# Performance work log

Measured on AMD Instinct MI355X. Metric: run time of the kernel, lower is better.

## Reference

```python
import jax, jax.numpy as jnp
import numpy as np

N_RAYS, N_SAMPLES, HIDDEN, N_VOXELS = 8192, 256, 64, 1000


def setup_inputs() -> dict:
    key = jax.random.key(0)
    ks = jax.random.split(key, 10)
    ray_start = jax.random.normal(ks[0], (N_RAYS, 3), jnp.float32)
    ray_dir = jax.random.normal(ks[1], (N_RAYS, 3), jnp.float32)
    ray_dir = ray_dir / jnp.linalg.norm(ray_dir, axis=-1, keepdims=True)
    # monotonically increasing depths along each ray
    sampled_depth = jnp.sort(jax.random.uniform(ks[2], (N_RAYS, N_SAMPLES), jnp.float32) * 4.0 + 0.5, axis=-1)
    sampled_dists = jax.random.uniform(ks[3], (N_RAYS, N_SAMPLES), jnp.float32) * 0.02 + 1e-3
    sampled_idx = jax.random.randint(ks[4], (N_RAYS, N_SAMPLES), -333, N_VOXELS).astype(jnp.int64)
    W1 = jax.random.normal(ks[5], (3, HIDDEN), jnp.float32) * 0.5
    b1 = jnp.zeros((HIDDEN,), jnp.float32)
    w_sigma = jax.random.normal(ks[6], (HIDDEN,), jnp.float32) * 0.5
    W_rgb = jax.random.normal(ks[7], (HIDDEN, 3), jnp.float32) * 0.5
    W_dir = jax.random.normal(ks[8], (3, 3), jnp.float32) * 0.5
    b_rgb = jnp.zeros((3,), jnp.float32)
    return {"ray_start": ray_start, "ray_dir": ray_dir, "sampled_depth": sampled_depth,
            "sampled_dists": sampled_dists, "sampled_idx": sampled_idx,
            "W1": W1, "b1": b1, "w_sigma": w_sigma, "W_rgb": W_rgb, "W_dir": W_dir, "b_rgb": b_rgb}


def _volume_render(ray_start, ray_dir, sampled_depth, sampled_dists, sampled_idx,
                   W1, b1, w_sigma, W_rgb, W_dir, b_rgb):
    # sampled_xyz = ray(ray_start, ray_dir, depth)
    xyz = ray_start[:, None, :] + ray_dir[:, None, :] * sampled_depth[..., None]  # [N,P,3]
    h = jax.nn.relu(jnp.einsum('npi,ih->nph', xyz, W1) + b1)                      # [N,P,H]
    sigma = jnp.einsum('nph,h->np', h, w_sigma)                                   # [N,P]
    rgb = jax.nn.sigmoid(jnp.einsum('nph,hc->npc', h, W_rgb)
                         + jnp.einsum('ni,ic->nc', ray_dir, W_dir)[:, None, :] + b_rgb)  # [N,P,3]
    mask = (sampled_idx != -1).astype(sigma.dtype)                                # [N,P]
    # free_energy = relu(sigma) * dists * 7.0, scattered back with zeros at misses
    free_energy = jax.nn.relu(sigma) * sampled_dists * 7.0 * mask
    shifted = jnp.concatenate([jnp.zeros_like(free_energy[:, :1]), free_energy[:, :-1]], axis=-1)
    a = 1.0 - jnp.exp(-free_energy)
    b = jnp.exp(-jnp.cumsum(shifted, axis=-1))
    probs = a * b                                                                 # [N,P]
    depths = jnp.sum(sampled_depth * probs, axis=-1)                              # [N]
    missed = 1.0 - jnp.sum(probs, axis=-1)                                        # [N]
    colors = jnp.sum(rgb * probs[..., None], axis=-2)                             # [N,3]
    return jnp.concatenate([colors, depths[:, None], missed[:, None], probs], axis=-1)  # [N, 3+1+1+P]


def reference(ray_start, ray_dir, sampled_depth, sampled_dists, sampled_idx,
              W1, b1, w_sigma, W_rgb, W_dir, b_rgb):
    return _volume_render(ray_start, ray_dir, sampled_depth, sampled_dists, sampled_idx,
                          W1, b1, w_sigma, W_rgb, W_dir, b_rgb)
```

## Files before the change

### kernel.cpp

```cpp
#include <hip/hip_runtime.h>

#define NRAYS 8192
#define NS    256
#define HID   64
#define NPAIR 32
#define RPB   8

typedef _Float16 f16x2 __attribute__((ext_vector_type(2)));
typedef _Float16 f16x8 __attribute__((ext_vector_type(8)));
typedef float    f32x4 __attribute__((ext_vector_type(4)));

static __device__ __forceinline__ f16x2 mk2(float a, float b) {
    f16x2 v; v.x = (_Float16)a; v.y = (_Float16)b; return v;
}

struct __align__(8) AB2 { f16x2 A, B; };
union AFrag { f16x8 v; f16x2 h[4]; };

__global__ __launch_bounds__(256, 4) void vr_kernel(
    const float* __restrict__ ray_start,
    const float* __restrict__ ray_dir,
    const float* __restrict__ sampled_depth,
    const float* __restrict__ sampled_dists,
    const int*   __restrict__ sampled_idx,
    const float* __restrict__ W1,
    const float* __restrict__ b1,
    const float* __restrict__ w_sigma,
    const float* __restrict__ W_rgb,
    const float* __restrict__ W_dir,
    const float* __restrict__ b_rgb,
    float* __restrict__ out)
{
    __shared__ AB2   sAB[RPB][NPAIR];
    __shared__ f16x2 sDep[RPB][NS];
    __shared__ __align__(16) float sOut[4][4][264];

    const int t = threadIdx.x;

    {
        const int rr  = t >> 5;
        const int k   = t & (NPAIR - 1);
        const int ray = blockIdx.x * RPB + rr;
        const float ox = ray_start[ray*3+0], oy = ray_start[ray*3+1], oz = ray_start[ray*3+2];
        const float dx = ray_dir[ray*3+0],  dy = ray_dir[ray*3+1],  dz = ray_dir[ray*3+2];
        const int h0 = 2*k, h1 = 2*k + 1;
        const float u0 = W1[h0], u1 = W1[HID + h0], u2 = W1[2*HID + h0];
        const float v0 = W1[h1], v1 = W1[HID + h1], v2 = W1[2*HID + h1];
        const float A0 = fmaf(u0, ox, fmaf(u1, oy, fmaf(u2, oz, b1[h0])));
        const float B0 = fmaf(u0, dx, fmaf(u1, dy, u2 * dz));
        const float A1 = fmaf(v0, ox, fmaf(v1, oy, fmaf(v2, oz, b1[h1])));
        const float B1 = fmaf(v0, dx, fmaf(v1, dy, v2 * dz));
        AB2 e; e.A = mk2(A0, A1); e.B = mk2(B0, B1);
        sAB[rr][k] = e;
    }
    {
        const int rr  = t >> 5;
        const int i   = t & 31;
        const int ray = blockIdx.x * RPB + rr;
        const size_t base = (size_t)ray * NS + (size_t)i * 8;
        const float4 d0 = ((const float4*)(sampled_depth + base))[0];
        const float4 d1 = ((const float4*)(sampled_depth + base))[1];
        f16x2* dst = &sDep[rr][i*8];
        dst[0] = mk2(d0.x, d0.x); dst[1] = mk2(d0.y, d0.y);
        dst[2] = mk2(d0.z, d0.z); dst[3] = mk2(d0.w, d0.w);
        dst[4] = mk2(d1.x, d1.x); dst[5] = mk2(d1.y, d1.y);
        dst[6] = mk2(d1.z, d1.z); dst[7] = mk2(d1.w, d1.w);
    }

    const int lane = t & 63;
    const int wave = t >> 6;
    const int col  = lane & 15;
    const int g    = lane >> 4;

    f16x8 bf0, bf1;
#pragma unroll
    for (int e = 0; e < 8; ++e) {
        const int u0 = g*8 + e, u1 = 32 + g*8 + e;
        float v0 = 0.f, v1 = 0.f;
        if (col == 0)     { v0 = w_sigma[u0];           v1 = w_sigma[u1]; }
        else if (col < 4) { v0 = W_rgb[u0*3 + (col-1)]; v1 = W_rgb[u1*3 + (col-1)]; }
        bf0[e] = (_Float16)v0; bf1[e] = (_Float16)v1;
    }

    const f16x2 zero2 = mk2(0.f, 0.f);
    const f32x4 zacc  = {0.f, 0.f, 0.f, 0.f};
    const int sb = 4*lane;

#pragma unroll 1
    for (int q = 0; q < 2; ++q) {
        const int r   = wave*2 + q;
        const int ray = blockIdx.x * RPB + r;

        AB2 c0[4], c1[4];
#pragma unroll
        for (int d = 0; d < 4; ++d) {
            c0[d] = sAB[r][4*g + d];
            c1[d] = sAB[r][16 + 4*g + d];
        }

        const float ddx = ray_dir[ray*3+0], ddy = ray_dir[ray*3+1], ddz = ray_dir[ray*3+2];
        const float dwr = fmaf(ddx, W_dir[0], fmaf(ddy, W_dir[3], fmaf(ddz, W_dir[6], b_rgb[0])));
        const float dwg = fmaf(ddx, W_dir[1], fmaf(ddy, W_dir[4], fmaf(ddz, W_dir[7], b_rgb[1])));
        const float dwb = fmaf(ddx, W_dir[2], fmaf(ddy, W_dir[5], fmaf(ddz, W_dir[8], b_rgb[2])));

        float4 dpt, dsv; int4 vid;

#pragma unroll
        for (int p = 0; p < 2; ++p) {
            f32x4 acc[8];
#pragma unroll
            for (int b = 0; b < 8; ++b) acc[b] = zacc;

#pragma unroll
            for (int b = 0; b < 8; ++b) {
                const int bb = 8*p + b;
                const f16x2 t2 = sDep[r][16*bb + col];
                AFrag a0, a1;
#pragma unroll
                for (int d = 0; d < 4; ++d) {
                    a0.h[d] = __builtin_elementwise_max(
                        __builtin_elementwise_fma(c0[d].B, t2, c0[d].A), zero2);
                    a1.h[d] = __builtin_elementwise_max(
                        __builtin_elementwise_fma(c1[d].B, t2, c1[d].A), zero2);
                }
                acc[b] = __builtin_amdgcn_mfma_f32_16x16x32_f16(a0.v, bf0, acc[b], 0, 0, 0);
                acc[b] = __builtin_amdgcn_mfma_f32_16x16x32_f16(a1.v, bf1, acc[b], 0, 0, 0);
            }

            if (col < 4) {
#pragma unroll
                for (int b = 0; b < 8; ++b) {
                    const int bb = 8*p + b;
                    float4 v; v.x = acc[b][0]; v.y = acc[b][1]; v.z = acc[b][2]; v.w = acc[b][3];
                    *(float4*)&sOut[wave][col][16*bb + 4*g] = v;
                }
            }

            if (p == 0) {
                const size_t rb = (size_t)ray * NS + (size_t)sb;
                dpt = *(const float4*)(sampled_depth + rb);
                dsv = *(const float4*)(sampled_dists + rb);
                vid = *(const int4*)(sampled_idx + rb);
            }
        }

        const float4 sg  = *(const float4*)&sOut[wave][0][sb];
        const float4 cr4 = *(const float4*)&sOut[wave][1][sb];
        const float4 cg4 = *(const float4*)&sOut[wave][2][sb];
        const float4 cb4 = *(const float4*)&sOut[wave][3][sb];

        const float sigA[4] = {sg.x,  sg.y,  sg.z,  sg.w};
        const float crA[4]  = {cr4.x, cr4.y, cr4.z, cr4.w};
        const float cgA[4]  = {cg4.x, cg4.y, cg4.z, cg4.w};
        const float cbA[4]  = {cb4.x, cb4.y, cb4.z, cb4.w};
        const float dptA[4] = {dpt.x, dpt.y, dpt.z, dpt.w};
        const float dsvA[4] = {dsv.x, dsv.y, dsv.z, dsv.w};
        const int   vidA[4] = {vid.x, vid.y, vid.z, vid.w};

        float c[4]; float run = 0.f;
#pragma unroll
        for (int j = 0; j < 4; ++j) {
            float f = fmaxf(sigA[j], 0.f) * dsvA[j] * 7.0f;
            if (vidA[j] == -1) f = 0.f;
            run += f; c[j] = run;
        }

        float tot = run;
#pragma unroll
        for (int off = 1; off < 64; off <<= 1) {
            const float v = __shfl_up(tot, off, 64);
            if (lane >= off) tot += v;
        }
        const float base = tot - run;

        float Eprev = __expf(-base);
        float prob[4];
        float sS = 0.f, sD = 0.f, sR = 0.f, sG = 0.f, sB = 0.f;
#pragma unroll
        for (int j = 0; j < 4; ++j) {
            const float Ej = __expf(-(base + c[j]));
            const float p  = Eprev - Ej;
            Eprev = Ej;
            prob[j] = p;
            const float rr2 = __builtin_amdgcn_rcpf(1.f + __expf(-(crA[j] + dwr)));
            const float gg2 = __builtin_amdgcn_rcpf(1.f + __expf(-(cgA[j] + dwg)));
            const float bb2 = __builtin_amdgcn_rcpf(1.f + __expf(-(cbA[j] + dwb)));
            sS += p;
            sD = fmaf(dptA[j], p, sD);
            sR = fmaf(rr2, p, sR);
            sG = fmaf(gg2, p, sG);
            sB = fmaf(bb2, p, sB);
        }

#pragma unroll
        for (int off = 32; off >= 1; off >>= 1) {
            sS += __shfl_xor(sS, off);
            sD += __shfl_xor(sD, off);
            sR += __shfl_xor(sR, off);
            sG += __shfl_xor(sG, off);
            sB += __shfl_xor(sB, off);
        }

        float* orow = out + (size_t)ray * (NS + 5);
#pragma unroll
        for (int j = 0; j < 4; ++j)
            orow[5 + sb + j] = prob[j];

        if (lane == 0) {
            orow[0] = sR;
            orow[1] = sG;
            orow[2] = sB;
            orow[3] = sD;
            orow[4] = 1.f - sS;
        }
    }
}

extern "C" void kernel_launch(void* const* d_in, const int* in_sizes, int n_in,
                              void* d_out, int out_size, void* d_ws, size_t ws_size,
                              hipStream_t stream)
{
    vr_kernel<<<NRAYS / RPB, 256, 0, stream>>>(
        (const float*)d_in[0],
        (const float*)d_in[1],
        (const float*)d_in[2],
        (const float*)d_in[3],
        (const int*)  d_in[4],
        (const float*)d_in[5],
        (const float*)d_in[6],
        (const float*)d_in[7],
        (const float*)d_in[8],
        (const float*)d_in[9],
        (const float*)d_in[10],
        (float*)d_out);
}
```

Baseline: 100.8 us.

## Merge per-ray epilogues into one half-wave-per-ray pass after both MFMA phases

Each wave now runs the MFMA phase for both of its rays first and keeps both results in a doubled shared output buffer. It then does a single epilogue in which each half-wave handles one ray with 8 samples per lane, so the scan and reduction use 32-lane shuffles. This removes one serialized epilogue per wave and halves the shuffle depth. Depth is stored in shared memory as packed f16 and broadcast in registers, and the per-ray direction term is computed once up front. The cost is more shared memory and more registers, which can lower occupancy.

New measurement: 100.7 us. Within noise of the previous version (-0.1%).

```diff
diff --git a/kernel.cpp b/kernel.cpp
--- a/kernel.cpp
+++ b/kernel.cpp
@@ -31,9 +31,9 @@
     const float* __restrict__ b_rgb,
     float* __restrict__ out)
 {
-    __shared__ AB2   sAB[RPB][NPAIR];
-    __shared__ f16x2 sDep[RPB][NS];
-    __shared__ __align__(16) float sOut[4][4][264];
+    __shared__ AB2 sAB[RPB][NPAIR];
+    __shared__ __align__(16) _Float16 sDepF[RPB][NS];
+    __shared__ __align__(16) float sOut[4][2][4][264];
 
     const int t = threadIdx.x;
 
@@ -60,17 +60,22 @@
         const size_t base = (size_t)ray * NS + (size_t)i * 8;
         const float4 d0 = ((const float4*)(sampled_depth + base))[0];
         const float4 d1 = ((const float4*)(sampled_depth + base))[1];
-        f16x2* dst = &sDep[rr][i*8];
-        dst[0] = mk2(d0.x, d0.x); dst[1] = mk2(d0.y, d0.y);
-        dst[2] = mk2(d0.z, d0.z); dst[3] = mk2(d0.w, d0.w);
-        dst[4] = mk2(d1.x, d1.x); dst[5] = mk2(d1.y, d1.y);
-        dst[6] = mk2(d1.z, d1.z); dst[7] = mk2(d1.w, d1.w);
+        f16x8 pk;
+        pk[0] = (_Float16)d0.x; pk[1] = (_Float16)d0.y;
+        pk[2] = (_Float16)d0.z; pk[3] = (_Float16)d0.w;
+        pk[4] = (_Float16)d1.x; pk[5] = (_Float16)d1.y;
+        pk[6] = (_Float16)d1.z; pk[7] = (_Float16)d1.w;
+        *(f16x8*)&sDepF[rr][i*8] = pk;
     }
 
     const int lane = t & 63;
     const int wave = t >> 6;
     const int col  = lane & 15;
     const int g    = lane >> 4;
+
+    const int hl   = lane & 31;
+    const int rq   = lane >> 5;
+    const int eray = blockIdx.x * RPB + wave*2 + rq;
 
     f16x8 bf0, bf1;
 #pragma unroll
@@ -82,14 +87,21 @@
         bf0[e] = (_Float16)v0; bf1[e] = (_Float16)v1;
     }
 
+    float dwr, dwg, dwb;
+    {
+        const float ddx = ray_dir[eray*3+0], ddy = ray_dir[eray*3+1], ddz = ray_dir[eray*3+2];
+        dwr = fmaf(ddx, W_dir[0], fmaf(ddy, W_dir[3], fmaf(ddz, W_dir[6], b_rgb[0])));
+        dwg = fmaf(ddx, W_dir[1], fmaf(ddy, W_dir[4], fmaf(ddz, W_dir[7], b_rgb[1])));
+        dwb = fmaf(ddx, W_dir[2], fmaf(ddy, W_dir[5], fmaf(ddz, W_dir[8], b_rgb[2])));
+    }
+
     const f16x2 zero2 = mk2(0.f, 0.f);
     const f32x4 zacc  = {0.f, 0.f, 0.f, 0.f};
-    const int sb = 4*lane;
-
-#pragma unroll 1
-    for (int q = 0; q < 2; ++q) {
-        const int r   = wave*2 + q;
-        const int ray = blockIdx.x * RPB + r;
+
+    float4 dptE0, dptE1, dsvE0, dsvE1; int4 vidE0, vidE1;
+
+    auto run_main = [&](int q, bool pf) {
+        const int r = wave*2 + q;
 
         AB2 c0[4], c1[4];
 #pragma unroll
@@ -98,12 +110,7 @@
             c1[d] = sAB[r][16 + 4*g + d];
         }
 
-        const float ddx = ray_dir[ray*3+0], ddy = ray_dir[ray*3+1], ddz = ray_dir[ray*3+2];
-        const float dwr = fmaf(ddx, W_dir[0], fmaf(ddy, W_dir[3], fmaf(ddz, W_dir[6], b_rgb[0])));
-        const float dwg = fmaf(ddx, W_dir[1], fmaf(ddy, W_dir[4], fmaf(ddz, W_dir[7], b_rgb[1])));
-        const float dwb = fmaf(ddx, W_dir[2], fmaf(ddy, W_dir[5], fmaf(ddz, W_dir[8], b_rgb[2])));
-
-        float4 dpt, dsv; int4 vid;
+        const unsigned short* sd = (const unsigned short*)sDepF[r];
 
 #pragma unroll
         for (int p = 0; p < 2; ++p) {
@@ -114,7 +121,9 @@
 #pragma unroll
             for (int b = 0; b < 8; ++b) {
                 const int bb = 8*p + b;
-                const f16x2 t2 = sDep[r][16*bb + col];
+                const unsigned int raw = sd[16*bb + col];
+                const unsigned int bits = (raw << 16) | raw;
+                const f16x2 t2 = __builtin_bit_cast(f16x2, bits);
                 AFrag a0, a1;
 #pragma unroll
                 for (int d = 0; d < 4; ++d) {
@@ -132,87 +141,98 @@
                 for (int b = 0; b < 8; ++b) {
                     const int bb = 8*p + b;
                     float4 v; v.x = acc[b][0]; v.y = acc[b][1]; v.z = acc[b][2]; v.w = acc[b][3];
-                    *(float4*)&sOut[wave][col][16*bb + 4*g] = v;
+                    *(float4*)&sOut[wave][q][col][16*bb + 4*g] = v;
                 }
             }
 
-            if (p == 0) {
-                const size_t rb = (size_t)ray * NS + (size_t)sb;
-                dpt = *(const float4*)(sampled_depth + rb);
-                dsv = *(const float4*)(sampled_dists + rb);
-                vid = *(const int4*)(sampled_idx + rb);
+            if (pf && p == 0) {
+                const size_t erb = (size_t)eray * NS + (size_t)hl * 8;
+                dptE0 = ((const float4*)(sampled_depth + erb))[0];
+                dptE1 = ((const float4*)(sampled_depth + erb))[1];
+                dsvE0 = ((const float4*)(sampled_dists + erb))[0];
+                dsvE1 = ((const float4*)(sampled_dists + erb))[1];
+                vidE0 = ((const int4*)(sampled_idx + erb))[0];
+                vidE1 = ((const int4*)(sampled_idx + erb))[1];
             }
         }
-
-        const float4 sg  = *(const float4*)&sOut[wave][0][sb];
-        const float4 cr4 = *(const float4*)&sOut[wave][1][sb];
-        const float4 cg4 = *(const float4*)&sOut[wave][2][sb];
-        const float4 cb4 = *(const float4*)&sOut[wave][3][sb];
-
-        const float sigA[4] = {sg.x,  sg.y,  sg.z,  sg.w};
-        const float crA[4]  = {cr4.x, cr4.y, cr4.z, cr4.w};
-        const float cgA[4]  = {cg4.x, cg4.y, cg4.z, cg4.w};
-        const float cbA[4]  = {cb4.x, cb4.y, cb4.z, cb4.w};
-        const float dptA[4] = {dpt.x, dpt.y, dpt.z, dpt.w};
-        const float dsvA[4] = {dsv.x, dsv.y, dsv.z, dsv.w};
-        const int   vidA[4] = {vid.x, vid.y, vid.z, vid.w};
-
-        float c[4]; float run = 0.f;
-#pragma unroll
-        for (int j = 0; j < 4; ++j) {
-            float f = fmaxf(sigA[j], 0.f) * dsvA[j] * 7.0f;
-            if (vidA[j] == -1) f = 0.f;
-            run += f; c[j] = run;
-        }
-
-        float tot = run;
-#pragma unroll
-        for (int off = 1; off < 64; off <<= 1) {
-            const float v = __shfl_up(tot, off, 64);
-            if (lane >= off) tot += v;
-        }
-        const float base = tot - run;
-
-        float Eprev = __expf(-base);
-        float prob[4];
-        float sS = 0.f, sD = 0.f, sR = 0.f, sG = 0.f, sB = 0.f;
-#pragma unroll
-        for (int j = 0; j < 4; ++j) {
-            const float Ej = __expf(-(base + c[j]));
-            const float p  = Eprev - Ej;
-            Eprev = Ej;
-            prob[j] = p;
-            const float rr2 = __builtin_amdgcn_rcpf(1.f + __expf(-(crA[j] + dwr)));
-            const float gg2 = __builtin_amdgcn_rcpf(1.f + __expf(-(cgA[j] + dwg)));
-            const float bb2 = __builtin_amdgcn_rcpf(1.f + __expf(-(cbA[j] + dwb)));
-            sS += p;
-            sD = fmaf(dptA[j], p, sD);
-            sR = fmaf(rr2, p, sR);
-            sG = fmaf(gg2, p, sG);
-            sB = fmaf(bb2, p, sB);
-        }
-
-#pragma unroll
-        for (int off = 32; off >= 1; off >>= 1) {
-            sS += __shfl_xor(sS, off);
-            sD += __shfl_xor(sD, off);
-            sR += __shfl_xor(sR, off);
-            sG += __shfl_xor(sG, off);
-            sB += __shfl_xor(sB, off);
-        }
-
-        float* orow = out + (size_t)ray * (NS + 5);
-#pragma unroll
-        for (int j = 0; j < 4; ++j)
-            orow[5 + sb + j] = prob[j];
-
-        if (lane == 0) {
-            orow[0] = sR;
-            orow[1] = sG;
-            orow[2] = sB;
-            orow[3] = sD;
-            orow[4] = 1.f - sS;
-        }
+    };
+
+    run_main(0, false);
+    run_main(1, true);
+
+    const int sb = 8*hl;
+    const float4 sg0 = *(const float4*)&sOut[wave][rq][0][sb];
+    const float4 sg1 = *(const float4*)&sOut[wave][rq][0][sb+4];
+    const float4 cr0 = *(const float4*)&sOut[wave][rq][1][sb];
+    const float4 cr1 = *(const float4*)&sOut[wave][rq][1][sb+4];
+    const float4 cg0 = *(const float4*)&sOut[wave][rq][2][sb];
+    const float4 cg1 = *(const float4*)&sOut[wave][rq][2][sb+4];
+    const float4 cb0 = *(const float4*)&sOut[wave][rq][3][sb];
+    const float4 cb1 = *(const float4*)&sOut[wave][rq][3][sb+4];
+
+    const float sigA[8] = {sg0.x, sg0.y, sg0.z, sg0.w, sg1.x, sg1.y, sg1.z, sg1.w};
+    const float crA[8]  = {cr0.x, cr0.y, cr0.z, cr0.w, cr1.x, cr1.y, cr1.z, cr1.w};
+    const float cgA[8]  = {cg0.x, cg0.y, cg0.z, cg0.w, cg1.x, cg1.y, cg1.z, cg1.w};
+    const float cbA[8]  = {cb0.x, cb0.y, cb0.z, cb0.w, cb1.x, cb1.y, cb1.z, cb1.w};
+    const float dptA[8] = {dptE0.x, dptE0.y, dptE0.z, dptE0.w, dptE1.x, dptE1.y, dptE1.z, dptE1.w};
+    const float dsvA[8] = {dsvE0.x, dsvE0.y, dsvE0.z, dsvE0.w, dsvE1.x, dsvE1.y, dsvE1.z, dsvE1.w};
+    const int   vidA[8] = {vidE0.x, vidE0.y, vidE0.z, vidE0.w, vidE1.x, vidE1.y, vidE1.z, vidE1.w};
+
+    float c[8]; float run = 0.f;
+#pragma unroll
+    for (int j = 0; j < 8; ++j) {
+        float f = fmaxf(sigA[j], 0.f) * dsvA[j] * 7.0f;
+        if (vidA[j] == -1) f = 0.f;
+        run += f; c[j] = run;
+    }
+
+    float tot = run;
+#pragma unroll
+    for (int off = 1; off < 32; off <<= 1) {
+        const float v = __shfl_up(tot, off, 32);
+        if (hl >= off) tot += v;
+    }
+    const float base = tot - run;
+
+    float Eprev = __expf(-base);
+    float prob[8];
+    float sS = 0.f, sD = 0.f, sR = 0.f, sG = 0.f, sB = 0.f;
+#pragma unroll
+    for (int j = 0; j < 8; ++j) {
+        const float Ej = __expf(-(base + c[j]));
+        const float p  = Eprev - Ej;
+        Eprev = Ej;
+        prob[j] = p;
+        const float rr2 = __builtin_amdgcn_rcpf(1.f + __expf(-(crA[j] + dwr)));
+        const float gg2 = __builtin_amdgcn_rcpf(1.f + __expf(-(cgA[j] + dwg)));
+        const float bb2 = __builtin_amdgcn_rcpf(1.f + __expf(-(cbA[j] + dwb)));
+        sS += p;
+        sD = fmaf(dptA[j], p, sD);
+        sR = fmaf(rr2, p, sR);
+        sG = fmaf(gg2, p, sG);
+        sB = fmaf(bb2, p, sB);
+    }
+
+#pragma unroll
+    for (int off = 16; off >= 1; off >>= 1) {
+        sS += __shfl_xor(sS, off, 32);
+        sD += __shfl_xor(sD, off, 32);
+        sR += __shfl_xor(sR, off, 32);
+        sG += __shfl_xor(sG, off, 32);
+        sB += __shfl_xor(sB, off, 32);
+    }
+
+    float* orow = out + (size_t)eray * (NS + 5);
+#pragma unroll
+    for (int j = 0; j < 8; ++j)
+        orow[5 + sb + j] = prob[j];
+
+    if (hl == 0) {
+        orow[0] = sR;
+        orow[1] = sG;
+        orow[2] = sB;
+        orow[3] = sD;
+        orow[4] = 1.f - sS;
     }
 }
 
```
